# Kernel tuning notes

Hardware: AMD Instinct MI355X
Metric: run time of the kernel (lower is better)

Reference implementation:

```python
import jax, jax.numpy as jnp
import numpy as np

B, G, P, H = 32, 5000, 5000, 64
N = B * G
E_CO, E_GG = 1600000, 100000

def _bn(x, g, b):
    # BatchNorm1d in training mode: biased batch stats, eps=1e-5
    m = x.mean(0); v = x.var(0)
    return g * (x - m) * jax.lax.rsqrt(v + 1e-5) + b

def _renorm(t):
    # nn.Embedding(max_norm=True) -> rows renormed to L2 norm <= 1
    n = jnp.linalg.norm(t, axis=1, keepdims=True)
    return t * jnp.minimum(1.0, 1.0 / jnp.maximum(n, 1e-12))

def _sgconv(x, src, dst, w, W, b):
    # SGConv(K=1): gcn_norm (self-loops w=1, symmetric deg norm) spmm, then Linear
    n = x.shape[0]
    sl = jnp.arange(n)
    s = jnp.concatenate([src, sl]); d = jnp.concatenate([dst, sl])
    ww = jnp.concatenate([w, jnp.ones((n,), x.dtype)])
    deg = jax.ops.segment_sum(ww, d, num_segments=n)
    dinv = jnp.where(deg > 0, jax.lax.rsqrt(deg), 0.0)
    coef = dinv[s] * ww * dinv[d]
    agg = jax.ops.segment_sum(coef[:, None] * x[s], d, num_segments=n)
    return agg @ W.T + b

def _mlp3(x, W, b, g, bt):
    # MLP([h,h,h]): Lin-BN-ReLU-Lin-BN (trailing ReLU stripped by [:-1])
    h = jax.nn.relu(_bn(x @ W[0].T + b[0], g[0], bt[0]))
    return _bn(h @ W[1].T + b[1], g[1], bt[1])

def _gears(x, pert_idx, ei_co, w_co, ei_go, w_go, ei_bg, w_bg,
           gene_tab, pos_tab, go_tab, bg_tab, bn_g, bn_b, sg_W, sg_b,
           mlp_W, mlp_b, mlp_g, mlp_bt,
           rec_W1, rec_b1, rec_g1, rec_bt1, rec_W2, rec_b2, rec_g2, rec_bt2,
           indv_w1, indv_b1,
           cg_W1, cg_b1, cg_g1, cg_bt1, cg_W2, cg_b2, cg_g2, cg_bt2,
           indv_w2, indv_b2):
    nb = pert_idx.shape[0]
    ng = gene_tab.shape[0]
    emb = jnp.tile(_renorm(gene_tab), (nb, 1))                     # [B*G,H]
    base = jax.nn.relu(_bn(emb, bn_g[0], bn_b[0]))                 # bn_emb + emb_trans
    pos = jnp.tile(_renorm(pos_tab), (nb, 1))
    pos = _sgconv(pos, ei_co[0], ei_co[1], w_co, sg_W[0], sg_b[0]) # 1 gene-pos GNN layer, no trailing relu
    base = base + 0.2 * pos
    base = _mlp3(base, mlp_W[1], mlp_b[1], mlp_g[1], mlp_bt[1])    # emb_trans_v2
    pgo = _sgconv(_renorm(go_tab), ei_go[0], ei_go[1], w_go, sg_W[1], sg_b[1])
    pbg = _sgconv(_renorm(bg_tab), ei_bg[0], ei_bg[1], w_bg, sg_W[2], sg_b[2])
    pglob = _mlp3(pgo + pbg, mlp_W[0], mlp_b[0], mlp_g[0], mlp_bt[0])  # pert_emb_comb_trans
    base = base.reshape(nb, ng, -1)
    # one valid pert per graph -> pert_track reduces to a gather; pert_fuse then broadcast-add
    emb_total = _mlp3(pglob[pert_idx], mlp_W[2], mlp_b[2], mlp_g[2], mlp_bt[2])  # [B,H]
    base = base + emb_total[:, None, :]
    base = base.reshape(nb * ng, -1)
    base = jax.nn.relu(_bn(base, bn_g[1], bn_b[1]))                # bn_pert_base + transform
    h = jax.nn.relu(_bn(base @ rec_W1.T + rec_b1, rec_g1, rec_bt1))
    out = _bn(h @ rec_W2.T + rec_b2, rec_g2, rec_bt2).reshape(nb, ng, -1)
    w1 = jnp.einsum('bgh,gh->bg', out, indv_w1) + indv_b1          # per-gene decoder 1
    cg = jax.nn.relu(_bn(w1 @ cg_W1.T + cg_b1, cg_g1, cg_bt1))
    cg = _bn(cg @ cg_W2.T + cg_b2, cg_g2, cg_bt2)                  # cross_gene_state [B,H]
    cat = jnp.concatenate([w1[..., None], jnp.broadcast_to(cg[:, None, :], (nb, ng, cg.shape[-1]))], -1)
    out2 = jnp.einsum('bgk,gk->bg', cat, indv_w2) + indv_b2        # per-gene decoder 2
    return out2 + x.reshape(nb, ng)

def setup_inputs():
    ks = jax.random.split(jax.random.key(0), 48)
    rn = lambda i, sh, s=0.05: jax.random.normal(ks[i], sh, jnp.float32) * s
    return {
        "x": rn(0, (N,), 1.0),
        "pert_idx": jax.random.randint(ks[1], (B,), 0, P),
        "ei_co": jax.random.randint(ks[2], (2, E_CO), 0, N),
        "w_co": jax.random.uniform(ks[3], (E_CO,), jnp.float32),
        "ei_go": jax.random.randint(ks[4], (2, E_GG), 0, P),
        "w_go": jax.random.uniform(ks[5], (E_GG,), jnp.float32),
        "ei_bg": jax.random.randint(ks[6], (2, E_GG), 0, P),
        "w_bg": jax.random.uniform(ks[7], (E_GG,), jnp.float32),
        "gene_tab": rn(8, (G, H), 1.0),
        "pos_tab": rn(9, (G, H), 1.0),
        "go_tab": rn(10, (P, H), 1.0),
        "bg_tab": rn(11, (P, H), 1.0),
        "bn_g": jnp.ones((2, H)), "bn_b": jnp.zeros((2, H)),
        "sg_W": rn(12, (3, H, H)), "sg_b": jnp.zeros((3, H)),
        "mlp_W": rn(13, (3, 2, H, H)), "mlp_b": jnp.zeros((3, 2, H)),
        "mlp_g": jnp.ones((3, 2, H)), "mlp_bt": jnp.zeros((3, 2, H)),
        "rec_W1": rn(14, (2 * H, H)), "rec_b1": jnp.zeros((2 * H,)),
        "rec_g1": jnp.ones((2 * H,)), "rec_bt1": jnp.zeros((2 * H,)),
        "rec_W2": rn(15, (H, 2 * H)), "rec_b2": jnp.zeros((H,)),
        "rec_g2": jnp.ones((H,)), "rec_bt2": jnp.zeros((H,)),
        "indv_w1": rn(16, (G, H)), "indv_b1": rn(17, (G,)),
        "cg_W1": rn(18, (H, G), 0.01), "cg_b1": jnp.zeros((H,)),
        "cg_g1": jnp.ones((H,)), "cg_bt1": jnp.zeros((H,)),
        "cg_W2": rn(19, (H, H)), "cg_b2": jnp.zeros((H,)),
        "cg_g2": jnp.ones((H,)), "cg_bt2": jnp.zeros((H,)),
        "indv_w2": rn(20, (G, H + 1)), "indv_b2": rn(21, (G,)),
    }

def reference(x, pert_idx, ei_co, w_co, ei_go, w_go, ei_bg, w_bg,
              gene_tab, pos_tab, go_tab, bg_tab, bn_g, bn_b, sg_W, sg_b,
              mlp_W, mlp_b, mlp_g, mlp_bt,
              rec_W1, rec_b1, rec_g1, rec_bt1, rec_W2, rec_b2, rec_g2, rec_bt2,
              indv_w1, indv_b1,
              cg_W1, cg_b1, cg_g1, cg_bt1, cg_W2, cg_b2, cg_g2, cg_bt2,
              indv_w2, indv_b2):
    return _gears(x, pert_idx, ei_co, w_co, ei_go, w_go, ei_bg, w_bg,
                  gene_tab, pos_tab, go_tab, bg_tab, bn_g, bn_b, sg_W, sg_b,
                  mlp_W, mlp_b, mlp_g, mlp_bt,
                  rec_W1, rec_b1, rec_g1, rec_bt1, rec_W2, rec_b2, rec_g2, rec_bt2,
                  indv_w1, indv_b1,
                  cg_W1, cg_b1, cg_g1, cg_bt1, cg_W2, cg_b2, cg_g2, cg_bt2,
                  indv_w2, indv_b2)
```

## Files before the change

### kernel.cpp

```cpp
#include <hip/hip_runtime.h>

typedef unsigned int u32;
typedef unsigned short u16;

constexpr int Gn  = 5000;
constexpr int Bn  = 32;
constexpr int Pn  = 5000;
constexpr int Nn  = Bn * Gn;
constexpr int ECO = 1600000;
constexpr int EGG = 100000;
constexpr int NTILES = Nn / 128;
constexpr int PTILES = 40;
constexpr int NBK = 625;

constexpr int oS1 = 0, oS2 = 128, oS3 = 256, oS4 = 384, oS5 = 640, oSG = 768, oSP1 = 896, oSP2 = 1024;
constexpr int oZERO = 1536;
constexpr int oA1 = 2048, oB1 = 2112, oA2 = 2176, oB2 = 2240;
constexpr int oA4 = 2304, oB4 = 2432;
constexpr int oA5 = 2560, oB5 = 2624;
constexpr int oAG = 2688, oBG = 2752;
constexpr int oAP1 = 2816, oBP1 = 2880, oAP2 = 2944, oBP2 = 3008;
constexpr int oAvec = 3072, oCvec = 3136, oCcP = 3200;
constexpr int oM  = 4096, oM1 = 8192;
constexpr int oE2 = 16384, oEMB = 18432, oCGRAW = 20480, oCG2 = 22528;
constexpr int oRG  = 24576;
constexpr int oRP  = oRG  + Gn * 64;
constexpr int oQ   = oRP  + Gn * 64;
constexpr int oRGO = oQ   + Gn * 64;
constexpr int oRBG = oRGO + Pn * 64;
constexpr int oAGO = oRBG + Pn * 64;
constexpr int oABG = oAGO + Pn * 64;
constexpr int oM1B = oABG + Pn * 64;
constexpr int oM2B = oM1B + Pn * 64;
constexpr int oDGO = oM2B + Pn * 64;
constexpr int oDBG = oDGO + Pn;
constexpr int oDEG = oDBG + Pn;
constexpr int oW1  = oDEG + Nn;
constexpr int oBUF0 = oW1 + Nn;
constexpr int oBUF1 = oBUF0 + Nn * 64;
constexpr size_t WS_FLOATS = (size_t)oBUF1 + (size_t)Nn * 64;

__device__ inline u16 f2bf(float f) {
  u32 u = __float_as_uint(f);
  u = (u + 0x7fffu + ((u >> 16) & 1u)) >> 16;
  return (u16)u;
}
__device__ inline float bflo(u32 v) { return __uint_as_float(v << 16); }
__device__ inline float bfhi(u32 v) { return __uint_as_float(v & 0xffff0000u); }
__device__ inline float bf2f(u16 v) { return __uint_as_float((u32)v << 16); }

typedef __attribute__((ext_vector_type(8))) short short8v;
typedef __attribute__((ext_vector_type(4))) float f32x4;

__global__ __launch_bounds__(256) void kzero(float* p, int n) {
  int i = blockIdx.x * 256 + threadIdx.x;
  if (i < n) p[i] = 0.f;
}

__global__ __launch_bounds__(256) void krenorm(const float* __restrict__ in, float* __restrict__ out,
                                               float* __restrict__ stats, u16* __restrict__ outb, int rows) {
  int lane = threadIdx.x & 63, wv = threadIdx.x >> 6;
  int gw = blockIdx.x * 4 + wv, nw = gridDim.x * 4;
  float ps = 0.f, pq = 0.f;
  for (int r = gw; r < rows; r += nw) {
    float v = in[r * 64 + lane];
    float sq = v * v;
    for (int off = 32; off; off >>= 1) sq += __shfl_xor(sq, off, 64);
    float nn = sqrtf(sq);
    float s = fminf(1.f, 1.f / fmaxf(nn, 1e-12f));
    float o = v * s;
    out[r * 64 + lane] = o;
    if (outb) outb[r * 64 + lane] = f2bf(o);
    ps += o; pq += o * o;
  }
  if (!stats) return;
  __shared__ float red[4][64], red2[4][64];
  red[wv][lane] = ps; red2[wv][lane] = pq;
  __syncthreads();
  if (wv == 0) {
    float s = red[0][lane] + red[1][lane] + red[2][lane] + red[3][lane];
    float q = red2[0][lane] + red2[1][lane] + red2[2][lane] + red2[3][lane];
    atomicAdd(&stats[lane], s);
    atomicAdd(&stats[64 + lane], q);
  }
}

__global__ void kfin(const float* __restrict__ stats, const float* __restrict__ g,
                     const float* __restrict__ bt, float* __restrict__ a, float* __restrict__ b,
                     int cols, float invn) {
  int c = blockIdx.x * 64 + threadIdx.x;
  if (c >= cols) return;
  float mean = stats[c] * invn;
  float var = stats[cols + c] * invn - mean * mean;
  float sc = g[c] * rsqrtf(var + 1e-5f);
  a[c] = sc;
  b[c] = bt[c] - mean * sc;
}

__global__ __launch_bounds__(256) void ksmallmat(const float* __restrict__ A, const float* __restrict__ Bm,
                                                 float alpha, const float* __restrict__ bias,
                                                 const float* __restrict__ bv1, const float* __restrict__ bv2,
                                                 float beta, float* __restrict__ Mout, int mpitch,
                                                 float* __restrict__ cvec) {
  __shared__ float As[4096], Bs[4096];
  int t = threadIdx.x;
  for (int m = 0; m < 16; m++) { As[m * 256 + t] = A[m * 256 + t]; Bs[m * 256 + t] = Bm[m * 256 + t]; }
  __syncthreads();
  int j = t & 63, ig = t >> 6;
  for (int ii = 0; ii < 16; ii++) {
    int i = ig * 16 + ii;
    float acc = 0.f;
    for (int k = 0; k < 64; k++) acc += As[i * 64 + k] * Bs[k * 64 + j];
    Mout[i * mpitch + j] = alpha * acc;
  }
  if (cvec && t < 64) {
    float acc = bias ? bias[t] : 0.f;
    for (int k = 0; k < 64; k++) {
      float bb = (bv1 ? bv1[k] : 0.f) + (bv2 ? bv2[k] : 0.f);
      acc += beta * As[t * 64 + k] * bb;
    }
    cvec[t] = acc;
  }
}

__global__ __launch_bounds__(256) void khist(const int* __restrict__ dst, int* __restrict__ cnt,
                                             int* __restrict__ ticket, int E) {
  int e = blockIdx.x * 256 + threadIdx.x;
  if (e < E) ticket[e] = atomicAdd(&cnt[dst[e]], 1);
}

__global__ __launch_bounds__(256) void kscan1(const int* __restrict__ cnt, int* __restrict__ bsum, int n) {
  __shared__ int sh[256];
  int b = blockIdx.x, t = threadIdx.x;
  int base = b * 1024 + t * 4;
  int s = 0;
#pragma unroll
  for (int j = 0; j < 4; j++) { int i = base + j; if (i < n) s += cnt[i]; }
  sh[t] = s; __syncthreads();
  for (int d = 128; d; d >>= 1) { if (t < d) sh[t] += sh[t + d]; __syncthreads(); }
  if (t == 0) bsum[b] = sh[0];
}
__global__ __launch_bounds__(256) void kscan2(int* bsum, int nb, int* off_n) {
  __shared__ int sh[256];
  int t = threadIdx.x;
  int v = (t < nb) ? bsum[t] : 0;
  sh[t] = v;
  __syncthreads();
  for (int d = 1; d < 256; d <<= 1) {
    int u = (t >= d) ? sh[t - d] : 0;
    __syncthreads();
    sh[t] += u;
    __syncthreads();
  }
  if (t < nb) bsum[t] = sh[t] - v;
  if (t == nb - 1 && off_n) *off_n = sh[t];
}
__global__ __launch_bounds__(256) void kscan3(int* __restrict__ cnt, const int* __restrict__ bsum, int n) {
  __shared__ int sh[256];
  int b = blockIdx.x, t = threadIdx.x;
  int base = b * 1024 + t * 4;
  int c0 = (base + 0 < n) ? cnt[base + 0] : 0;
  int c1 = (base + 1 < n) ? cnt[base + 1] : 0;
  int c2 = (base + 2 < n) ? cnt[base + 2] : 0;
  int c3 = (base + 3 < n) ? cnt[base + 3] : 0;
  int tot = c0 + c1 + c2 + c3;
  sh[t] = tot; __syncthreads();
  for (int d = 1; d < 256; d <<= 1) {
    int v = (t >= d) ? sh[t - d] : 0;
    __syncthreads();
    sh[t] += v;
    __syncthreads();
  }
  int excl = sh[t] - tot + bsum[b];
  if (base + 0 < n) cnt[base + 0] = excl;
  if (base + 1 < n) cnt[base + 1] = excl + c0;
  if (base + 2 < n) cnt[base + 2] = excl + c0 + c1;
  if (base + 3 < n) cnt[base + 3] = excl + c0 + c1 + c2;
}

__global__ __launch_bounds__(256) void kfillt(const int* __restrict__ src, const int* __restrict__ dst,
                                              const float* __restrict__ w, const int* __restrict__ off,
                                              const int* __restrict__ ticket, float2* __restrict__ pack, int E) {
  int e = blockIdx.x * 256 + threadIdx.x;
  if (e >= E) return;
  int d = dst[e];
  int pos = off[d] + ticket[e];
  pack[pos] = make_float2(w[e], __int_as_float(src[e]));
}

__global__ __launch_bounds__(256) void kdinvrow(const int* __restrict__ off, const float2* __restrict__ pack,
                                                float* __restrict__ dinv, int n) {
  int i = blockIdx.x * 256 + threadIdx.x;
  if (i >= n) return;
  int b0 = off[i], b1 = off[i + 1];
  float s = 1.f;
  for (int j = b0; j < b1; j++) s += pack[j].x;
  dinv[i] = rsqrtf(s);
}

__global__ __launch_bounds__(256) void kpcnt(const int* __restrict__ dst, int* __restrict__ bcnt, int E) {
  __shared__ int h[NBK];
  int t = threadIdx.x;
  for (int i = t; i < NBK; i += 256) h[i] = 0;
  __syncthreads();
  int stride = gridDim.x * 256;
  for (int e = blockIdx.x * 256 + t; e < E; e += stride) atomicAdd(&h[dst[e] >> 8], 1);
  __syncthreads();
  for (int i = t; i < NBK; i += 256) { int c = h[i]; if (c) atomicAdd(&bcnt[i], c); }
}
__global__ __launch_bounds__(256) void kpscan(const int* __restrict__ bcnt, int* __restrict__ bbase,
                                              int* __restrict__ bcur, int* __restrict__ offN) {
  __shared__ int sh[256];
  int t = threadIdx.x;
  int i0 = t * 3;
  int c[3];
  int s = 0;
#pragma unroll
  for (int j = 0; j < 3; j++) { int i = i0 + j; c[j] = (i < NBK) ? bcnt[i] : 0; s += c[j]; }
  sh[t] = s;
  __syncthreads();
  for (int d = 1; d < 256; d <<= 1) {
    int u = (t >= d) ? sh[t - d] : 0;
    __syncthreads();
    sh[t] += u;
    __syncthreads();
  }
  int base = sh[t] - s;
#pragma unroll
  for (int j = 0; j < 3; j++) {
    int i = i0 + j;
    if (i < NBK) { bbase[i] = base; bcur[i] = base; }
    base += c[j];
  }
  if (t == 255) { bbase[NBK] = base; *offN = base; }
}
__global__ __launch_bounds__(256) void kpscat(const int* __restrict__ src, const int* __restrict__ dst,
                                              const float* __restrict__ w, int* __restrict__ bcur,
                                              float2* __restrict__ sa, u16* __restrict__ sb, int E) {
  __shared__ int h[NBK];
  int t = threadIdx.x;
  constexpr int EPB = (ECO + 255) / 256;
  int e0 = blockIdx.x * EPB;
  int e1 = e0 + EPB; if (e1 > E) e1 = E;
  for (int i = t; i < NBK; i += 256) h[i] = 0;
  __syncthreads();
  for (int e = e0 + t; e < e1; e += 256) atomicAdd(&h[dst[e] >> 8], 1);
  __syncthreads();
  for (int i = t; i < NBK; i += 256) {
    int c = h[i];
    h[i] = c ? atomicAdd(&bcur[i], c) : 0;
  }
  __syncthreads();
  for (int e = e0 + t; e < e1; e += 256) {
    int d = dst[e];
    int pos = atomicAdd(&h[d >> 8], 1);
    sa[pos] = make_float2(w[e], __int_as_float(src[e]));
    sb[pos] = (u16)(d & 255);
  }
}
__global__ __launch_bounds__(256) void kpcsr(const int* __restrict__ bbase, const float2* __restrict__ sa,
                                             const u16* __restrict__ sb, int* __restrict__ off,
                                             float2* __restrict__ pack, float* __restrict__ dinv) {
  __shared__ int rh[256];
  __shared__ int sc[256];
  __shared__ float ws[256];
  int bk = blockIdx.x, t = threadIdx.x;
  int s0 = bbase[bk], s1 = bbase[bk + 1];
  rh[t] = 0; ws[t] = 0.f;
  __syncthreads();
  for (int i = s0 + t; i < s1; i += 256) {
    int r = sb[i];
    atomicAdd(&rh[r], 1);
    atomicAdd(&ws[r], sa[i].x);
  }
  __syncthreads();
  int cnt = rh[t];
  sc[t] = cnt;
  __syncthreads();
  for (int d = 1; d < 256; d <<= 1) {
    int u = (t >= d) ? sc[t - d] : 0;
    __syncthreads();
    sc[t] += u;
    __syncthreads();
  }
  int gpos = s0 + sc[t] - cnt;
  int grow = (bk << 8) + t;
  off[grow] = gpos;
  dinv[grow] = rsqrtf(1.f + ws[t]);
  rh[t] = gpos;
  __syncthreads();
  for (int i = s0 + t; i < s1; i += 256) {
    int pos = atomicAdd(&rh[sb[i]], 1);
    pack[pos] = sa[i];
  }
}

__global__ __launch_bounds__(256) void kgather(const int* __restrict__ off, const float2* __restrict__ pack,
                                               const float* __restrict__ dinv, const float* __restrict__ tab,
                                               u16* __restrict__ aggb, int pitch, int coff, int n) {
  int lane = threadIdx.x & 63;
  int wv = blockIdx.x * 4 + (threadIdx.x >> 6);
  int nw = gridDim.x * 4;
  for (int i = wv; i < n; i += nw) {
    int b0 = off[i], b1 = off[i + 1];
    float di = dinv[i];
    float acc = di * tab[(i % Gn) * 64 + lane];
    for (int base = b0; base < b1; base += 64) {
      int m = b1 - base; if (m > 64) m = 64;
      float cj = 0.f; int idxj = 0;
      if (lane < m) {
        float2 p = pack[base + lane];
        int s = __float_as_int(p.y);
        cj = p.x * dinv[s];
        idxj = (s % Gn) * 64;
      }
      int j = 0;
      for (; j + 1 < m; j += 2) {
        float c0 = __shfl(cj, j, 64);     int i0 = __shfl(idxj, j, 64);
        float c1 = __shfl(cj, j + 1, 64); int i1 = __shfl(idxj, j + 1, 64);
        float t0 = tab[i0 + lane];
        float t1 = tab[i1 + lane];
        acc = fmaf(c0, t0, acc);
        acc = fmaf(c1, t1, acc);
      }
      if (j < m) {
        float c0 = __shfl(cj, j, 64); int i0 = __shfl(idxj, j, 64);
        acc = fmaf(c0, tab[i0 + lane], acc);
      }
    }
    acc *= di;
    aggb[(size_t)i * pitch + coff + lane] = f2bf(acc);
  }
}

template <int K, int OUTC, bool PRE, bool EB, bool PERG, bool STATS, bool OUTF32, bool STATB>
__global__ __launch_bounds__(256, 3) void mfgemm(
    const u16* __restrict__ Xb, const float* __restrict__ Wg, const float* __restrict__ bias,
    const float* __restrict__ pa, const float* __restrict__ pb,
    const float* __restrict__ perg, u16* __restrict__ Ybf, float* __restrict__ stats,
    float* __restrict__ statB, int rows) {
  constexpr int NT  = OUTC / 16;
  constexpr int KH  = K / 32;
  constexpr int SLK = K / 8;
  constexpr int SLO = OUTC / 8;
  constexpr int XROW = (K > OUTC ? K : OUTC) * 2;
  __shared__ __align__(16) unsigned char xsb[128 * XROW];
  __shared__ __align__(16) unsigned char wsb[OUTC * K * 2];
  __shared__ float sstat[STATS ? 2 * OUTC : 1];
  __shared__ float sstatB[STATB ? 128 : 1];
  int t = threadIdx.x;
  int l = t & 63, w = t >> 6, lrow = l & 15, lk = l >> 4;
  int R0 = blockIdx.x * 128;

  for (int idx = t; idx < OUTC * SLK; idx += 256) {
    int oc = idx / SLK, s8 = idx % SLK;
    const float* wp = &Wg[oc * K + s8 * 8];
    uint4 o;
    o.x = (u32)f2bf(wp[0]) | ((u32)f2bf(wp[1]) << 16);
    o.y = (u32)f2bf(wp[2]) | ((u32)f2bf(wp[3]) << 16);
    o.z = (u32)f2bf(wp[4]) | ((u32)f2bf(wp[5]) << 16);
    o.w = (u32)f2bf(wp[6]) | ((u32)f2bf(wp[7]) << 16);
    *(uint4*)&wsb[oc * (2 * K) + ((s8 * 16) ^ ((oc & 7) << 4))] = o;
  }
  if constexpr (STATS) for (int idx = t; idx < 2 * OUTC; idx += 256) sstat[idx] = 0.f;
  if constexpr (STATB) for (int idx = t; idx < 128; idx += 256) sstatB[idx] = 0.f;

#pragma unroll
  for (int m = 0; m < SLK / 2; m++) {
    int f = m * 256 + t;
    int r = f / SLK, s8 = f % SLK;
    uint4 u = *(const uint4*)&Xb[(size_t)(R0 + r) * K + s8 * 8];
    if constexpr (PRE) {
      int c0 = s8 * 8;
      float4 A0 = *(const float4*)&pa[c0];
      float4 A1 = *(const float4*)&pa[c0 + 4];
      const float* pbb = EB ? &pb[((R0 + r) / Gn) * 64] : pb;
      float4 B0 = *(const float4*)&pbb[c0];
      float4 B1 = *(const float4*)&pbb[c0 + 4];
      float v0 = fmaxf(fmaf(A0.x, bflo(u.x), B0.x), 0.f);
      float v1 = fmaxf(fmaf(A0.y, bfhi(u.x), B0.y), 0.f);
      float v2 = fmaxf(fmaf(A0.z, bflo(u.y), B0.z), 0.f);
      float v3 = fmaxf(fmaf(A0.w, bfhi(u.y), B0.w), 0.f);
      float v4 = fmaxf(fmaf(A1.x, bflo(u.z), B1.x), 0.f);
      float v5 = fmaxf(fmaf(A1.y, bfhi(u.z), B1.y), 0.f);
      float v6 = fmaxf(fmaf(A1.z, bflo(u.w), B1.z), 0.f);
      float v7 = fmaxf(fmaf(A1.w, bfhi(u.w), B1.w), 0.f);
      u.x = (u32)f2bf(v0) | ((u32)f2bf(v1) << 16);
      u.y = (u32)f2bf(v2) | ((u32)f2bf(v3) << 16);
      u.z = (u32)f2bf(v4) | ((u32)f2bf(v5) << 16);
      u.w = (u32)f2bf(v6) | ((u32)f2bf(v7) << 16);
    }
    *(uint4*)&xsb[r * XROW + ((s8 * 16) ^ ((r & 7) << 4))] = u;
  }
  float bcol[NT];
#pragma unroll
  for (int nt = 0; nt < NT; nt++) bcol[nt] = bias[nt * 16 + lrow];
  __syncthreads();

  short8v af[2][KH];
#pragma unroll
  for (int rt = 0; rt < 2; rt++)
#pragma unroll
    for (int h = 0; h < KH; h++) {
      int row = w * 32 + rt * 16 + lrow;
      af[rt][h] = *(const short8v*)&xsb[row * XROW + ((h * 64 + lk * 16) ^ ((row & 7) << 4))];
    }
  f32x4 acc[2][NT];
#pragma unroll
  for (int rt = 0; rt < 2; rt++)
#pragma unroll
    for (int nt = 0; nt < NT; nt++) {
      f32x4 z = {0.f, 0.f, 0.f, 0.f};
      acc[rt][nt] = z;
    }
#pragma unroll
  for (int nt = 0; nt < NT; nt++) {
    int brow = nt * 16 + lrow;
#pragma unroll
    for (int h = 0; h < KH; h++) {
      short8v bfr = *(const short8v*)&wsb[brow * (2 * K) + ((h * 64 + lk * 16) ^ ((brow & 7) << 4))];
      acc[0][nt] = __builtin_amdgcn_mfma_f32_16x16x32_bf16(af[0][h], bfr, acc[0][nt], 0, 0, 0);
      acc[1][nt] = __builtin_amdgcn_mfma_f32_16x16x32_bf16(af[1][h], bfr, acc[1][nt], 0, 0, 0);
    }
  }
  __syncthreads();

  float sS[NT], sQ[NT], sB0[NT], sB1[NT];
#pragma unroll
  for (int nt = 0; nt < NT; nt++) { sS[nt] = 0.f; sQ[nt] = 0.f; sB0[nt] = 0.f; sB1[nt] = 0.f; }
  int hiStart = STATB ? (R0 / Gn + 1) * Gn : 0x7fffffff;
  float* Yf = (float*)Ybf;
#pragma unroll
  for (int rt = 0; rt < 2; rt++) {
#pragma unroll
    for (int r = 0; r < 4; r++) {
      int orow = w * 32 + rt * 16 + lk * 4 + r;
      int grow = R0 + orow;
      bool valid = grow < rows;
      int qoff = 0;
      if constexpr (PERG) qoff = (grow % Gn) * 64;
#pragma unroll
      for (int nt = 0; nt < NT; nt++) {
        float v = acc[rt][nt][r] + bcol[nt];
        if constexpr (PERG) v += perg[qoff + nt * 16 + lrow];
        if (valid) {
          if constexpr (STATS) { sS[nt] += v; sQ[nt] += v * v; }
          if constexpr (STATB) { if (grow >= hiStart) sB1[nt] += v; else sB0[nt] += v; }
        }
        if constexpr (OUTF32) {
          if (valid) Yf[(size_t)grow * OUTC + nt * 16 + lrow] = v;
        } else {
          *(u16*)&xsb[orow * (2 * OUTC) + ((2 * (nt * 16 + lrow)) ^ ((orow & 7) << 4))] = f2bf(v);
        }
      }
    }
  }
  if constexpr (STATS) {
#pragma unroll
    for (int nt = 0; nt < NT; nt++) {
      atomicAdd(&sstat[nt * 16 + lrow], sS[nt]);
      atomicAdd(&sstat[OUTC + nt * 16 + lrow], sQ[nt]);
    }
  }
  if constexpr (STATB) {
#pragma unroll
    for (int nt = 0; nt < NT; nt++) {
      atomicAdd(&sstatB[nt * 16 + lrow], sB0[nt]);
      atomicAdd(&sstatB[64 + nt * 16 + lrow], sB1[nt]);
    }
  }
  __syncthreads();

  if constexpr (!OUTF32) {
#pragma unroll
    for (int m = 0; m < SLO / 2; m++) {
      int f = m * 256 + t;
      int r = f / SLO, c8 = f % SLO;
      uint4 o = *(const uint4*)&xsb[r * (2 * OUTC) + ((16 * c8) ^ ((r & 7) << 4))];
      *(uint4*)&Ybf[(size_t)(R0 + r) * OUTC + c8 * 8] = o;
    }
  }
  if constexpr (STATS)
    for (int idx = t; idx < 2 * OUTC; idx += 256) atomicAdd(&stats[idx], sstat[idx]);
  if constexpr (STATB) {
    int bLo = R0 / Gn;
    for (int idx = t; idx < 128; idx += 256) {
      int b = bLo + (idx >> 6);
      if (b < Bn) atomicAdd(&statB[b * 64 + (idx & 63)], sstatB[idx]);
    }
  }
}

__global__ __launch_bounds__(256) void kfinS3e2(const float* __restrict__ S2, const float* __restrict__ g,
                                                const float* __restrict__ bt, const float* __restrict__ a2,
                                                const float* __restrict__ b2, const float* __restrict__ emb,
                                                const float* __restrict__ S3B,
                                                float* __restrict__ Avec, float* __restrict__ e2) {
  __shared__ float a3s[64], b3s[64];
  int t = threadIdx.x;
  if (t < 64) {
    float a2c = a2[t], b2c = b2[t];
    float su = 0.f, sxc = 0.f, sc2 = 0.f;
    for (int b = 0; b < Bn; b++) {
      float cb = b2c + emb[b * 64 + t];
      float sb = S3B[b * 64 + t];
      su += cb;
      sxc += cb * sb;
      sc2 += cb * cb;
    }
    float Su = a2c * S2[t] + (float)Gn * su;
    float Sq = a2c * a2c * S2[64 + t] + 2.f * a2c * sxc + (float)Gn * sc2;
    float mean = Su * (1.f / Nn);
    float var = Sq * (1.f / Nn) - mean * mean;
    float sc = g[t] * rsqrtf(var + 1e-5f);
    float sh = bt[t] - mean * sc;
    a3s[t] = sc; b3s[t] = sh;
    Avec[t] = sc * a2c;
  }
  __syncthreads();
  for (int idx = t; idx < 2048; idx += 256) {
    int c = idx & 63;
    e2[idx] = a3s[c] * (b2[c] + emb[idx]) + b3s[c];
  }
}

__global__ __launch_bounds__(256) void k13_kernel(const u16* __restrict__ R2, const float* __restrict__ a5,
                                                  const float* __restrict__ b5, const float* __restrict__ iw1,
                                                  const float* __restrict__ ib1, float* __restrict__ w1out,
                                                  int rows) {
  int t = blockIdx.x * 256 + threadIdx.x;
  int i = t >> 4, j = t & 15;
  if (i >= rows) return;
  int g = i % Gn;
  uint2 u = *(const uint2*)&R2[(size_t)i * 64 + j * 4];
  float rx = bflo(u.x), ry = bfhi(u.x), rz = bflo(u.y), rw = bfhi(u.y);
  float4 a = ((const float4*)a5)[j];
  float4 b = ((const float4*)b5)[j];
  float4 w = ((const float4*)iw1)[g * 16 + j];
  float p = (a.x * rx + b.x) * w.x + (a.y * ry + b.y) * w.y +
            (a.z * rz + b.z) * w.z + (a.w * rw + b.w) * w.w;
  for (int off = 8; off; off >>= 1) p += __shfl_xor(p, off, 64);
  if (j == 0) w1out[i] = p + ib1[g];
}

__global__ __launch_bounds__(256) void kinitcg(const float* __restrict__ cgb1, float* __restrict__ cgraw) {
  int idx = blockIdx.x * 256 + threadIdx.x;
  if (idx < Bn * 64) cgraw[idx] = cgb1[idx & 63];
}

__global__ __launch_bounds__(256) void kcg1s(const float* __restrict__ w1, const float* __restrict__ cgW1,
                                             float* __restrict__ cgraw) {
  __shared__ float w1s[64 * 36];
  __shared__ float cgs[64 * 65];
  int t = threadIdx.x;
  int k0 = blockIdx.x * 64;
  int kmax = Gn - k0; if (kmax > 64) kmax = 64;
  for (int idx = t; idx < 2048; idx += 256) {
    int row = idx >> 6, k = idx & 63;
    w1s[k * 36 + row] = (k < kmax) ? w1[row * Gn + k0 + k] : 0.f;
  }
  for (int idx = t; idx < 4096; idx += 256) {
    int col = idx >> 6, k = idx & 63;
    cgs[k * 65 + col] = (k < kmax) ? cgW1[col * Gn + k0 + k] : 0.f;
  }
  __syncthreads();
  int col = t & 63, rg = t >> 6;
  float acc[8];
#pragma unroll
  for (int i = 0; i < 8; i++) acc[i] = 0.f;
  for (int k = 0; k < 64; k++) {
    float wk = cgs[k * 65 + col];
    const float* wr = &w1s[k * 36 + rg * 8];
    float4 r0 = *(const float4*)wr;
    float4 r1 = *(const float4*)(wr + 4);
    acc[0] = fmaf(r0.x, wk, acc[0]);
    acc[1] = fmaf(r0.y, wk, acc[1]);
    acc[2] = fmaf(r0.z, wk, acc[2]);
    acc[3] = fmaf(r0.w, wk, acc[3]);
    acc[4] = fmaf(r1.x, wk, acc[4]);
    acc[5] = fmaf(r1.y, wk, acc[5]);
    acc[6] = fmaf(r1.z, wk, acc[6]);
    acc[7] = fmaf(r1.w, wk, acc[7]);
  }
#pragma unroll
  for (int i = 0; i < 8; i++) atomicAdd(&cgraw[(rg * 8 + i) * 64 + col], acc[i]);
}

__global__ __launch_bounds__(256) void kcg2(const float* __restrict__ cgraw, const float* __restrict__ g1,
                                            const float* __restrict__ bt1, const float* __restrict__ W2,
                                            const float* __restrict__ b2, const float* __restrict__ g2,
                                            const float* __restrict__ bt2, float* __restrict__ cg2out) {
  int t = threadIdx.x, c = t & 63, bg = t >> 6;
  __shared__ float hmid[2048], sred[4][64], qred[4][64], asc[64], bsh[64];
  float y[8];
  float ps = 0.f, pq = 0.f;
  for (int jb = 0; jb < 8; jb++) {
    int b = bg * 8 + jb;
    float v = cgraw[b * 64 + c];
    y[jb] = v; ps += v; pq += v * v;
  }
  sred[bg][c] = ps; qred[bg][c] = pq;
  __syncthreads();
  if (t < 64) {
    float s = sred[0][t] + sred[1][t] + sred[2][t] + sred[3][t];
    float q = qred[0][t] + qred[1][t] + qred[2][t] + qred[3][t];
    float mean = s * (1.f / 32.f), var = q * (1.f / 32.f) - mean * mean;
    float sc = g1[t] * rsqrtf(var + 1e-5f);
    asc[t] = sc; bsh[t] = bt1[t] - mean * sc;
  }
  __syncthreads();
  for (int jb = 0; jb < 8; jb++) { int b = bg * 8 + jb; hmid[b * 64 + c] = fmaxf(asc[c] * y[jb] + bsh[c], 0.f); }
  __syncthreads();
  ps = 0.f; pq = 0.f;
  for (int jb = 0; jb < 8; jb++) {
    int b = bg * 8 + jb;
    float a = b2[c];
    for (int k = 0; k < 64; k++) a += hmid[b * 64 + k] * W2[c * 64 + k];
    y[jb] = a; ps += a; pq += a * a;
  }
  sred[bg][c] = ps; qred[bg][c] = pq;
  __syncthreads();
  if (t < 64) {
    float s = sred[0][t] + sred[1][t] + sred[2][t] + sred[3][t];
    float q = qred[0][t] + qred[1][t] + qred[2][t] + qred[3][t];
    float mean = s * (1.f / 32.f), var = q * (1.f / 32.f) - mean * mean;
    float sc = g2[t] * rsqrtf(var + 1e-5f);
    asc[t] = sc; bsh[t] = bt2[t] - mean * sc;
  }
  __syncthreads();
  for (int jb = 0; jb < 8; jb++) { int b = bg * 8 + jb; cg2out[b * 64 + c] = asc[c] * y[jb] + bsh[c]; }
}

__global__ __launch_bounds__(256) void kemb(const u16* __restrict__ m2, const float* __restrict__ aP2,
                                            const float* __restrict__ bP2, const int* __restrict__ pidx,
                                            const float* __restrict__ Wm, const float* __restrict__ bv,
                                            const float* __restrict__ gg, const float* __restrict__ btv,
                                            float* __restrict__ emb) {
  int t = threadIdx.x, c = t & 63, bg = t >> 6;
  __shared__ float xin[2048], hmid[2048], sred[4][64], qred[4][64], asc[64], bsh[64];
  for (int idx = t; idx < 2048; idx += 256) {
    int b = idx >> 6, cc = idx & 63;
    xin[idx] = aP2[cc] * bf2f(m2[(size_t)pidx[b] * 64 + cc]) + bP2[cc];
  }
  __syncthreads();
  float y[8];
  float ps = 0.f, pq = 0.f;
  for (int jb = 0; jb < 8; jb++) {
    int b = bg * 8 + jb;
    float a = bv[c];
    for (int k = 0; k < 64; k++) a += xin[b * 64 + k] * Wm[c * 64 + k];
    y[jb] = a; ps += a; pq += a * a;
  }
  sred[bg][c] = ps; qred[bg][c] = pq;
  __syncthreads();
  if (t < 64) {
    float s = sred[0][t] + sred[1][t] + sred[2][t] + sred[3][t];
    float q = qred[0][t] + qred[1][t] + qred[2][t] + qred[3][t];
    float mean = s * (1.f / 32.f), var = q * (1.f / 32.f) - mean * mean;
    float sc = gg[t] * rsqrtf(var + 1e-5f);
    asc[t] = sc; bsh[t] = btv[t] - mean * sc;
  }
  __syncthreads();
  for (int jb = 0; jb < 8; jb++) { int b = bg * 8 + jb; hmid[b * 64 + c] = fmaxf(asc[c] * y[jb] + bsh[c], 0.f); }
  __syncthreads();
  ps = 0.f; pq = 0.f;
  for (int jb = 0; jb < 8; jb++) {
    int b = bg * 8 + jb;
    float a = bv[64 + c];
    for (int k = 0; k < 64; k++) a += hmid[b * 64 + k] * Wm[4096 + c * 64 + k];
    y[jb] = a; ps += a; pq += a * a;
  }
  sred[bg][c] = ps; qred[bg][c] = pq;
  __syncthreads();
  if (t < 64) {
    float s = sred[0][t] + sred[1][t] + sred[2][t] + sred[3][t];
    float q = qred[0][t] + qred[1][t] + qred[2][t] + qred[3][t];
    float mean = s * (1.f / 32.f), var = q * (1.f / 32.f) - mean * mean;
    float sc = gg[64 + t] * rsqrtf(var + 1e-5f);
    asc[t] = sc; bsh[t] = btv[64 + t] - mean * sc;
  }
  __syncthreads();
  for (int jb = 0; jb < 8; jb++) { int b = bg * 8 + jb; emb[b * 64 + c] = asc[c] * y[jb] + bsh[c]; }
}

__global__ __launch_bounds__(256) void kfinal(const float* __restrict__ w1, const float* __restrict__ cg2,
                                              const float* __restrict__ iw2, const float* __restrict__ ib2,
                                              const float* __restrict__ x, float* __restrict__ out) {
  __shared__ float iws[64 * 65], cgs[2048];
  int t = threadIdx.x;
  int g0 = blockIdx.x * 64;
  for (int idx = t; idx < 64 * 65; idx += 256) {
    int gi = g0 * 65 + idx;
    iws[idx] = (gi < Gn * 65) ? iw2[gi] : 0.f;
  }
  for (int idx = t; idx < 2048; idx += 256) cgs[idx] = cg2[idx];
  __syncthreads();
  int gl = t & 63, bg = t >> 6;
  int g = g0 + gl;
  if (g >= Gn) return;
  float bias = ib2[g];
  for (int jb = 0; jb < 8; jb++) {
    int b = bg * 8 + jb;
    float acc = w1[b * Gn + g] * iws[gl * 65] + bias;
    for (int k = 0; k < 64; k++) acc += cgs[b * 64 + k] * iws[gl * 65 + 1 + k];
    out[b * Gn + g] = acc + x[b * Gn + g];
  }
}

extern "C" void kernel_launch(void* const* d_in, const int* in_sizes, int n_in,
                              void* d_out, int out_size, void* d_ws, size_t ws_size,
                              hipStream_t stream) {
  (void)in_sizes; (void)n_in; (void)out_size;
  if (ws_size < WS_FLOATS * sizeof(float)) return;

  const float* x        = (const float*)d_in[0];
  const int*   pert_idx = (const int*)d_in[1];
  const int*   ei_co    = (const int*)d_in[2];
  const float* w_co     = (const float*)d_in[3];
  const int*   ei_go    = (const int*)d_in[4];
  const float* w_go     = (const float*)d_in[5];
  const int*   ei_bg    = (const int*)d_in[6];
  const float* w_bg     = (const float*)d_in[7];
  const float* gene_tab = (const float*)d_in[8];
  const float* pos_tab  = (const float*)d_in[9];
  const float* go_tab   = (const float*)d_in[10];
  const float* bg_tab   = (const float*)d_in[11];
  const float* bn_g     = (const float*)d_in[12];
  const float* bn_b     = (const float*)d_in[13];
  const float* sg_W     = (const float*)d_in[14];
  const float* sg_b     = (const float*)d_in[15];
  const float* mlp_W    = (const float*)d_in[16];
  const float* mlp_b    = (const float*)d_in[17];
  const float* mlp_g    = (const float*)d_in[18];
  const float* mlp_bt   = (const float*)d_in[19];
  const float* rec_W1   = (const float*)d_in[20];
  const float* rec_b1   = (const float*)d_in[21];
  const float* rec_g1   = (const float*)d_in[22];
  const float* rec_bt1  = (const float*)d_in[23];
  const float* rec_W2   = (const float*)d_in[24];
  const float* rec_b2   = (const float*)d_in[25];
  const float* rec_g2   = (const float*)d_in[26];
  const float* rec_bt2  = (const float*)d_in[27];
  const float* indv_w1  = (const float*)d_in[28];
  const float* indv_b1  = (const float*)d_in[29];
  const float* cg_W1    = (const float*)d_in[30];
  const float* cg_b1    = (const float*)d_in[31];
  const float* cg_g1    = (const float*)d_in[32];
  const float* cg_bt1   = (const float*)d_in[33];
  const float* cg_W2    = (const float*)d_in[34];
  const float* cg_b2    = (const float*)d_in[35];
  const float* cg_g2    = (const float*)d_in[36];
  const float* cg_bt2   = (const float*)d_in[37];
  const float* indv_w2  = (const float*)d_in[38];
  const float* indv_b2  = (const float*)d_in[39];

  float* W = (float*)d_ws;
  float* buf0 = W + oBUF0;
  float* buf1 = W + oBUF1;

  int*    co_off    = (int*)(buf1);
  int*    bbase     = (int*)(buf1 + 200000);
  int*    bcur      = (int*)(buf1 + 201000);
  int*    bcnt      = (int*)(buf1 + 202000);
  int*    sbsum     = (int*)(buf1 + 320128);
  float2* co_pack   = (float2*)(buf1 + 400000);
  int*    go_cnt    = (int*)(buf1 + 3700000);
  float2* go_pack   = (float2*)(buf1 + 3720000);
  int*    bg_cnt    = (int*)(buf1 + 4000000);
  float2* bg_pack   = (float2*)(buf1 + 4020000);
  u16*    co_sb     = (u16*)(buf1 + 4500000);
  int*    go_ticket = (int*)(buf1 + 6200000);
  int*    bg_ticket = (int*)(buf1 + 6400000);
  u16*    pgi       = (u16*)(buf1 + 6600000);
  u16*    RGB       = (u16*)(buf1 + 6800000);
  float2* co_sa     = (float2*)(buf1 + 6963840);

  kzero<<<8, 256, 0, stream>>>(W, 2048);
  kzero<<<8, 256, 0, stream>>>(W + oE2, 2048);
  kzero<<<15, 256, 0, stream>>>(buf1 + 6800000 + 160000, 3840);
  kzero<<<30, 256, 0, stream>>>(buf1 + 6600000 + 320000, 7680);
  krenorm<<<160, 256, 0, stream>>>(gene_tab, W + oRG, W + oSG, RGB, Gn);
  krenorm<<<160, 256, 0, stream>>>(pos_tab, W + oRP, nullptr, nullptr, Gn);
  krenorm<<<160, 256, 0, stream>>>(go_tab, W + oRGO, nullptr, nullptr, Pn);
  krenorm<<<160, 256, 0, stream>>>(bg_tab, W + oRBG, nullptr, nullptr, Pn);
  kfin<<<1, 64, 0, stream>>>(W + oSG, bn_g, bn_b, W + oAG, W + oBG, 64, 1.f / Gn);
  ksmallmat<<<1, 256, 0, stream>>>(mlp_W + 8192, sg_W, 0.2f, mlp_b + 128, sg_b, nullptr, 0.2f,
                                   W + oM, 64, W + oCvec);
  ksmallmat<<<1, 256, 0, stream>>>(mlp_W, sg_W + 4096, 1.f, nullptr, nullptr, nullptr, 0.f,
                                   W + oM1, 128, nullptr);
  ksmallmat<<<1, 256, 0, stream>>>(mlp_W, sg_W + 8192, 1.f, mlp_b, sg_b + 64, sg_b + 128, 1.f,
                                   W + oM1 + 64, 128, W + oCcP);
  mfgemm<64, 64, true, false, false, false, true, false><<<PTILES, 256, 0, stream>>>(
      RGB, mlp_W + 8192, W + oCvec, W + oAG, W + oBG, nullptr, (u16*)(W + oQ), nullptr, nullptr, Gn);

  kzero<<<(5001 + 255) / 256, 256, 0, stream>>>((float*)go_cnt, 5001);
  khist<<<(EGG + 255) / 256, 256, 0, stream>>>(ei_go + EGG, go_cnt, go_ticket, EGG);
  kscan1<<<5, 256, 0, stream>>>(go_cnt, sbsum, Pn);
  kscan2<<<1, 256, 0, stream>>>(sbsum, 5, go_cnt + Pn);
  kscan3<<<5, 256, 0, stream>>>(go_cnt, sbsum, Pn);
  kfillt<<<(EGG + 255) / 256, 256, 0, stream>>>(ei_go, ei_go + EGG, w_go, go_cnt, go_ticket, go_pack, EGG);
  kdinvrow<<<(Pn + 255) / 256, 256, 0, stream>>>(go_cnt, go_pack, W + oDGO, Pn);
  kgather<<<512, 256, 0, stream>>>(go_cnt, go_pack, W + oDGO, W + oRGO, pgi, 128, 0, Pn);

  kzero<<<(5001 + 255) / 256, 256, 0, stream>>>((float*)bg_cnt, 5001);
  khist<<<(EGG + 255) / 256, 256, 0, stream>>>(ei_bg + EGG, bg_cnt, bg_ticket, EGG);
  kscan1<<<5, 256, 0, stream>>>(bg_cnt, sbsum, Pn);
  kscan2<<<1, 256, 0, stream>>>(sbsum, 5, bg_cnt + Pn);
  kscan3<<<5, 256, 0, stream>>>(bg_cnt, sbsum, Pn);
  kfillt<<<(EGG + 255) / 256, 256, 0, stream>>>(ei_bg, ei_bg + EGG, w_bg, bg_cnt, bg_ticket, bg_pack, EGG);
  kdinvrow<<<(Pn + 255) / 256, 256, 0, stream>>>(bg_cnt, bg_pack, W + oDBG, Pn);
  kgather<<<512, 256, 0, stream>>>(bg_cnt, bg_pack, W + oDBG, W + oRBG, pgi, 128, 64, Pn);

  mfgemm<128, 64, false, false, false, true, false, false><<<PTILES, 256, 0, stream>>>(
      pgi, W + oM1, W + oCcP, nullptr, nullptr, nullptr, (u16*)(W + oM1B), W + oSP1, nullptr, Pn);
  kfin<<<1, 64, 0, stream>>>(W + oSP1, mlp_g, mlp_bt, W + oAP1, W + oBP1, 64, 1.f / Pn);
  mfgemm<64, 64, true, false, false, true, false, false><<<PTILES, 256, 0, stream>>>(
      (u16*)(W + oM1B), mlp_W + 4096, mlp_b + 64, W + oAP1, W + oBP1, nullptr,
      (u16*)(W + oM2B), W + oSP2, nullptr, Pn);
  kfin<<<1, 64, 0, stream>>>(W + oSP2, mlp_g + 64, mlp_bt + 64, W + oAP2, W + oBP2, 64, 1.f / Pn);
  kemb<<<1, 256, 0, stream>>>((u16*)(W + oM2B), W + oAP2, W + oBP2, pert_idx,
                              mlp_W + 16384, mlp_b + 256, mlp_g + 256, mlp_bt + 256, W + oEMB);

  kzero<<<3, 256, 0, stream>>>((float*)bcnt, NBK);
  kpcnt<<<256, 256, 0, stream>>>(ei_co + ECO, bcnt, ECO);
  kpscan<<<1, 256, 0, stream>>>(bcnt, bbase, bcur, co_off + Nn);
  kpscat<<<256, 256, 0, stream>>>(ei_co, ei_co + ECO, w_co, bcur, co_sa, co_sb, ECO);
  kpcsr<<<NBK, 256, 0, stream>>>(bbase, co_sa, co_sb, co_off, co_pack, W + oDEG);
  kgather<<<2048, 256, 0, stream>>>(co_off, co_pack, W + oDEG, W + oRP, (u16*)buf0, 64, 0, Nn);

  mfgemm<64, 64, false, false, true, true, false, false><<<NTILES, 256, 0, stream>>>(
      (const u16*)buf0, W + oM, W + oZERO, nullptr, nullptr, W + oQ, (u16*)buf1, W + oS1, nullptr, Nn);
  kfin<<<1, 64, 0, stream>>>(W + oS1, mlp_g + 128, mlp_bt + 128, W + oA1, W + oB1, 64, 1.f / Nn);
  mfgemm<64, 64, true, false, false, true, false, true><<<NTILES, 256, 0, stream>>>(
      (const u16*)buf1, mlp_W + 12288, mlp_b + 192, W + oA1, W + oB1, nullptr,
      (u16*)buf0, W + oS2, W + oE2, Nn);
  kfin<<<1, 64, 0, stream>>>(W + oS2, mlp_g + 192, mlp_bt + 192, W + oA2, W + oB2, 64, 1.f / Nn);
  kfinS3e2<<<1, 256, 0, stream>>>(W + oS2, bn_g + 64, bn_b + 64, W + oA2, W + oB2, W + oEMB,
                                  W + oE2, W + oAvec, W + oE2);
  mfgemm<64, 128, true, true, false, true, false, false><<<NTILES, 256, 0, stream>>>(
      (const u16*)buf0, rec_W1, rec_b1, W + oAvec, W + oE2, nullptr, (u16*)buf1, W + oS4, nullptr, Nn);
  kfin<<<2, 64, 0, stream>>>(W + oS4, rec_g1, rec_bt1, W + oA4, W + oB4, 128, 1.f / Nn);
  mfgemm<128, 64, true, false, false, true, false, false><<<NTILES, 256, 0, stream>>>(
      (const u16*)buf1, rec_W2, rec_b2, W + oA4, W + oB4, nullptr, (u16*)buf0, W + oS5, nullptr, Nn);
  kfin<<<1, 64, 0, stream>>>(W + oS5, rec_g2, rec_bt2, W + oA5, W + oB5, 64, 1.f / Nn);
  k13_kernel<<<(Nn * 16 + 255) / 256, 256, 0, stream>>>((const u16*)buf0, W + oA5, W + oB5, indv_w1, indv_b1,
                                                        W + oW1, Nn);
  kinitcg<<<8, 256, 0, stream>>>(cg_b1, W + oCGRAW);
  kcg1s<<<(Gn + 63) / 64, 256, 0, stream>>>(W + oW1, cg_W1, W + oCGRAW);
  kcg2<<<1, 256, 0, stream>>>(W + oCGRAW, cg_g1, cg_bt1, cg_W2, cg_b2, cg_g2, cg_bt2, W + oCG2);
  kfinal<<<(Gn + 63) / 64, 256, 0, stream>>>(W + oW1, W + oCG2, indv_w2, indv_b2, x, (float*)d_out);
}
```

Measured before the change: 694.6 us.

## Replace global-atomic bucket scatter with per-block local sort and gather CSR build

The co-expression edge CSR build now sorts each block's edge chunk by bucket in shared memory and writes it contiguously. The per-block bucket counts and offsets go to global arrays. A second kernel per bucket gathers the sub-runs from all 256 blocks into shared memory and builds the rows. This drops the separate count pass, the global atomics on bucket cursors and the scattered staging writes, and packs the row-within-bucket into the high bits of src so the u16 side array is no longer needed. The risks are heavy shared memory use (32KB edge buffer per block), the assumption that a bucket holds at most 4096 edges, and serial per-thread copy loops in kpcsr2.

```diff
diff --git a/kernel.cpp b/kernel.cpp
--- a/kernel.cpp
+++ b/kernel.cpp
@@ -12,6 +12,7 @@
 constexpr int NTILES = Nn / 128;
 constexpr int PTILES = 40;
 constexpr int NBK = 625;
+constexpr int EPB2 = ECO / 256;
 
 constexpr int oS1 = 0, oS2 = 128, oS3 = 256, oS4 = 384, oS5 = 640, oSG = 768, oSP1 = 896, oSP2 = 1024;
 constexpr int oZERO = 1536;
@@ -198,18 +199,64 @@
   dinv[i] = rsqrtf(s);
 }
 
-__global__ __launch_bounds__(256) void kpcnt(const int* __restrict__ dst, int* __restrict__ bcnt, int E) {
-  __shared__ int h[NBK];
+__global__ __launch_bounds__(256) void kpsort(const int* __restrict__ src, const int* __restrict__ dst,
+                                              const float* __restrict__ w, float2* __restrict__ stg,
+                                              int* __restrict__ Cg, int* __restrict__ Lg) {
+  __shared__ int cnt[NBK];
+  __shared__ int loff[NBK];
+  __shared__ int cur[NBK];
+  __shared__ int ssc[256];
+  __shared__ float2 sbuf[EPB2];
   int t = threadIdx.x;
-  for (int i = t; i < NBK; i += 256) h[i] = 0;
-  __syncthreads();
-  int stride = gridDim.x * 256;
-  for (int e = blockIdx.x * 256 + t; e < E; e += stride) atomicAdd(&h[dst[e] >> 8], 1);
-  __syncthreads();
-  for (int i = t; i < NBK; i += 256) { int c = h[i]; if (c) atomicAdd(&bcnt[i], c); }
-}
+  int e0 = blockIdx.x * EPB2;
+  for (int i = t; i < NBK; i += 256) cnt[i] = 0;
+  __syncthreads();
+  for (int e = e0 + t; e < e0 + EPB2; e += 256) atomicAdd(&cnt[dst[e] >> 8], 1);
+  __syncthreads();
+  int i0 = t * 3;
+  int c3[3];
+  int s = 0;
+#pragma unroll
+  for (int j = 0; j < 3; j++) { int i = i0 + j; c3[j] = (i < NBK) ? cnt[i] : 0; s += c3[j]; }
+  ssc[t] = s;
+  __syncthreads();
+  for (int d = 1; d < 256; d <<= 1) {
+    int u = (t >= d) ? ssc[t - d] : 0;
+    __syncthreads();
+    ssc[t] += u;
+    __syncthreads();
+  }
+  int base = ssc[t] - s;
+#pragma unroll
+  for (int j = 0; j < 3; j++) {
+    int i = i0 + j;
+    if (i < NBK) { loff[i] = base; cur[i] = base; }
+    base += c3[j];
+  }
+  __syncthreads();
+  for (int e = e0 + t; e < e0 + EPB2; e += 256) {
+    int d = dst[e];
+    int pos = atomicAdd(&cur[d >> 8], 1);
+    sbuf[pos] = make_float2(w[e], __int_as_float(src[e] | ((d & 255) << 18)));
+  }
+  __syncthreads();
+  for (int i = t; i < EPB2; i += 256) stg[(size_t)e0 + i] = sbuf[i];
+  for (int i = t; i < NBK; i += 256) {
+    Cg[blockIdx.x * NBK + i] = cnt[i];
+    Lg[blockIdx.x * NBK + i] = loff[i];
+  }
+}
+
+__global__ __launch_bounds__(256) void ksumT(const int* __restrict__ Cg, int* __restrict__ T) {
+  int bk = blockIdx.x * 256 + threadIdx.x;
+  if (bk >= NBK) return;
+  int s = 0;
+  for (int blk = 0; blk < 256; blk++) s += Cg[blk * NBK + bk];
+  T[bk] = s;
+}
+
 __global__ __launch_bounds__(256) void kpscan(const int* __restrict__ bcnt, int* __restrict__ bbase,
-                                              int* __restrict__ bcur, int* __restrict__ offN) {
+                                              int* __restrict__ offN) {
   __shared__ int sh[256];
   int t = threadIdx.x;
   int i0 = t * 3;
@@ -229,69 +276,70 @@
 #pragma unroll
   for (int j = 0; j < 3; j++) {
     int i = i0 + j;
-    if (i < NBK) { bbase[i] = base; bcur[i] = base; }
+    if (i < NBK) bbase[i] = base;
     base += c[j];
   }
   if (t == 255) { bbase[NBK] = base; *offN = base; }
 }
-__global__ __launch_bounds__(256) void kpscat(const int* __restrict__ src, const int* __restrict__ dst,
-                                              const float* __restrict__ w, int* __restrict__ bcur,
-                                              float2* __restrict__ sa, u16* __restrict__ sb, int E) {
-  __shared__ int h[NBK];
-  int t = threadIdx.x;
-  constexpr int EPB = (ECO + 255) / 256;
-  int e0 = blockIdx.x * EPB;
-  int e1 = e0 + EPB; if (e1 > E) e1 = E;
-  for (int i = t; i < NBK; i += 256) h[i] = 0;
-  __syncthreads();
-  for (int e = e0 + t; e < e1; e += 256) atomicAdd(&h[dst[e] >> 8], 1);
-  __syncthreads();
-  for (int i = t; i < NBK; i += 256) {
-    int c = h[i];
-    h[i] = c ? atomicAdd(&bcur[i], c) : 0;
-  }
-  __syncthreads();
-  for (int e = e0 + t; e < e1; e += 256) {
-    int d = dst[e];
-    int pos = atomicAdd(&h[d >> 8], 1);
-    sa[pos] = make_float2(w[e], __int_as_float(src[e]));
-    sb[pos] = (u16)(d & 255);
-  }
-}
-__global__ __launch_bounds__(256) void kpcsr(const int* __restrict__ bbase, const float2* __restrict__ sa,
-                                             const u16* __restrict__ sb, int* __restrict__ off,
-                                             float2* __restrict__ pack, float* __restrict__ dinv) {
+
+__global__ __launch_bounds__(256) void kpcsr2(const int* __restrict__ bbase, const int* __restrict__ Cg,
+                                              const int* __restrict__ Lg, const float2* __restrict__ stg,
+                                              int* __restrict__ off, float2* __restrict__ pack,
+                                              float* __restrict__ dinv) {
+  constexpr int CAP = 4096;
+  __shared__ float2 ebuf[CAP];
   __shared__ int rh[256];
-  __shared__ int sc[256];
+  __shared__ int sc2[256];
   __shared__ float ws[256];
+  __shared__ int nEs;
   int bk = blockIdx.x, t = threadIdx.x;
-  int s0 = bbase[bk], s1 = bbase[bk + 1];
+  int myC = Cg[t * NBK + bk];
+  int myL = Lg[t * NBK + bk];
+  sc2[t] = myC;
+  __syncthreads();
+  for (int d = 1; d < 256; d <<= 1) {
+    int u = (t >= d) ? sc2[t - d] : 0;
+    __syncthreads();
+    sc2[t] += u;
+    __syncthreads();
+  }
+  int myO = sc2[t] - myC;
+  if (t == 255) nEs = sc2[255];
   rh[t] = 0; ws[t] = 0.f;
   __syncthreads();
-  for (int i = s0 + t; i < s1; i += 256) {
-    int r = sb[i];
+  int nE = nEs;
+  {
+    const float2* sp = &stg[(size_t)t * EPB2 + myL];
+    for (int i = 0; i < myC; i++) ebuf[myO + i] = sp[i];
+  }
+  __syncthreads();
+  for (int i = t; i < nE; i += 256) {
+    float2 p = ebuf[i];
+    int r = (__float_as_int(p.y) >> 18) & 255;
     atomicAdd(&rh[r], 1);
-    atomicAdd(&ws[r], sa[i].x);
+    atomicAdd(&ws[r], p.x);
   }
   __syncthreads();
   int cnt = rh[t];
-  sc[t] = cnt;
+  sc2[t] = cnt;
   __syncthreads();
   for (int d = 1; d < 256; d <<= 1) {
-    int u = (t >= d) ? sc[t - d] : 0;
-    __syncthreads();
-    sc[t] += u;
-    __syncthreads();
-  }
-  int gpos = s0 + sc[t] - cnt;
+    int u = (t >= d) ? sc2[t - d] : 0;
+    __syncthreads();
+    sc2[t] += u;
+    __syncthreads();
+  }
+  int gpos = bbase[bk] + sc2[t] - cnt;
   int grow = (bk << 8) + t;
   off[grow] = gpos;
   dinv[grow] = rsqrtf(1.f + ws[t]);
   rh[t] = gpos;
   __syncthreads();
-  for (int i = s0 + t; i < s1; i += 256) {
-    int pos = atomicAdd(&rh[sb[i]], 1);
-    pack[pos] = sa[i];
+  for (int i = t; i < nE; i += 256) {
+    float2 p = ebuf[i];
+    int r = (__float_as_int(p.y) >> 18) & 255;
+    int pos = atomicAdd(&rh[r], 1);
+    pack[pos] = p;
   }
 }
 
@@ -310,7 +358,7 @@
       float cj = 0.f; int idxj = 0;
       if (lane < m) {
         float2 p = pack[base + lane];
-        int s = __float_as_int(p.y);
+        int s = __float_as_int(p.y) & 0x3FFFF;
         cj = p.x * dinv[s];
         idxj = (s % Gn) * 64;
       }
@@ -760,20 +808,20 @@
 
   int*    co_off    = (int*)(buf1);
   int*    bbase     = (int*)(buf1 + 200000);
-  int*    bcur      = (int*)(buf1 + 201000);
-  int*    bcnt      = (int*)(buf1 + 202000);
+  int*    Tbk       = (int*)(buf1 + 202000);
   int*    sbsum     = (int*)(buf1 + 320128);
   float2* co_pack   = (float2*)(buf1 + 400000);
   int*    go_cnt    = (int*)(buf1 + 3700000);
   float2* go_pack   = (float2*)(buf1 + 3720000);
   int*    bg_cnt    = (int*)(buf1 + 4000000);
   float2* bg_pack   = (float2*)(buf1 + 4020000);
-  u16*    co_sb     = (u16*)(buf1 + 4500000);
+  int*    Cg        = (int*)(buf1 + 4500000);
+  int*    Lg        = (int*)(buf1 + 4700000);
   int*    go_ticket = (int*)(buf1 + 6200000);
   int*    bg_ticket = (int*)(buf1 + 6400000);
   u16*    pgi       = (u16*)(buf1 + 6600000);
   u16*    RGB       = (u16*)(buf1 + 6800000);
-  float2* co_sa     = (float2*)(buf1 + 6963840);
+  float2* co_stg    = (float2*)(buf1 + 6963840);
 
   kzero<<<8, 256, 0, stream>>>(W, 2048);
   kzero<<<8, 256, 0, stream>>>(W + oE2, 2048);
@@ -821,11 +869,10 @@
   kemb<<<1, 256, 0, stream>>>((u16*)(W + oM2B), W + oAP2, W + oBP2, pert_idx,
                               mlp_W + 16384, mlp_b + 256, mlp_g + 256, mlp_bt + 256, W + oEMB);
 
-  kzero<<<3, 256, 0, stream>>>((float*)bcnt, NBK);
-  kpcnt<<<256, 256, 0, stream>>>(ei_co + ECO, bcnt, ECO);
-  kpscan<<<1, 256, 0, stream>>>(bcnt, bbase, bcur, co_off + Nn);
-  kpscat<<<256, 256, 0, stream>>>(ei_co, ei_co + ECO, w_co, bcur, co_sa, co_sb, ECO);
-  kpcsr<<<NBK, 256, 0, stream>>>(bbase, co_sa, co_sb, co_off, co_pack, W + oDEG);
+  kpsort<<<256, 256, 0, stream>>>(ei_co, ei_co + ECO, w_co, co_stg, Cg, Lg);
+  ksumT<<<3, 256, 0, stream>>>(Cg, Tbk);
+  kpscan<<<1, 256, 0, stream>>>(Tbk, bbase, co_off + Nn);
+  kpcsr2<<<NBK, 256, 0, stream>>>(bbase, Cg, Lg, co_stg, co_off, co_pack, W + oDEG);
   kgather<<<2048, 256, 0, stream>>>(co_off, co_pack, W + oDEG, W + oRP, (u16*)buf0, 64, 0, Nn);
 
   mfgemm<64, 64, false, false, true, true, false, false><<<NTILES, 256, 0, stream>>>(
```

Measured after the change: 729.2 us. 5.0% more time.
